# Kernel optimization log

Measured on AMD Instinct MI355X. Metric: run time of the kernel, lower is better.

## Reference

```python
import jax, jax.numpy as jnp
import numpy as np

NUM_CLASSES = 8
SCORE_T = 0.5
IOU_T = 0.5
POSE_HYPS = 10
MAX_DET = 100
B, A = 1, 4096


def _pairwise_iou(bx):
    # bx: (N,4) in (x1,y1,x2,y2); TF-style +1 pixel convention
    x1 = jnp.maximum(bx[:, None, 0], bx[None, :, 0])
    y1 = jnp.maximum(bx[:, None, 1], bx[None, :, 1])
    x2 = jnp.minimum(bx[:, None, 2], bx[None, :, 2])
    y2 = jnp.minimum(bx[:, None, 3], bx[None, :, 3])
    wid = x2 - x1 + 1.0
    hei = y2 - y1 + 1.0
    inter = wid * hei
    area = (bx[:, 2] - bx[:, 0] + 1.0) * (bx[:, 3] - bx[:, 1] + 1.0)
    den = area[:, None] + area[None, :] - inter
    ov = jnp.where(den == 0.0, 0.0, inter / jnp.where(den == 0.0, 1.0, den))  # divide_no_nan
    return jnp.where((wid <= 0.0) | (hei <= 0.0), 0.0, ov)


def _per_class(scores_c, boxes_c, poses_c, conf_c):
    # Fixed-shape re-expression of _filter_detections: instead of compacting the
    # boxes with score > threshold (dynamic shape), keep all N and mask invalid
    # boxes out of the overlap indicator. Relative ordering (which drives the
    # argmax tie-break and the ascending sort) is identical to the compacted
    # subset, so the math matches exactly.
    N = scores_c.shape[0]
    K = POSE_HYPS + 1
    valid = scores_c > SCORE_T
    m = jnp.sum(valid.astype(jnp.int32))  # number of selected boxes
    ov = _pairwise_iou(boxes_c)  # (N,N)
    ind = ((ov > IOU_T) & valid[:, None] & valid[None, :]).astype(jnp.float32)
    # scatter_nd: true_ov[argmax_col(row i), i] = max(row i); column i is unique per update
    max_col = jnp.argmax(ind, axis=1)
    true_ov = jnp.zeros_like(ind).at[max_col, jnp.arange(N)].add(jnp.max(ind, axis=1))
    bc = (1.0 - ov) * true_ov * conf_c[None, :]
    bc = jnp.where(bc == 0.0, 1000.0, bc)  # 1000 = sentinel for 'not a hypothesis'
    # Only the first min(pose_hyps+1, m) ascending-sorted entries per row survive the
    # sequence mask, so take the K smallest instead of a full argsort (same result;
    # top_k of the negation breaks ties by lowest index like a stable ascending sort).
    neg, args = jax.lax.top_k(-bc, K)
    svals = -neg  # (N,K) K smallest per row
    hyp = (jnp.arange(K) < jnp.minimum(K, m)).astype(jnp.float32)
    cmask = jnp.where(svals == 1000.0, 0.0, 1.0) * hyp[None, :]
    denom = jnp.sum(cmask, axis=1)  # (N,)
    safe = jnp.where(denom == 0.0, 1.0, denom)
    poses_avg = jnp.where(denom[:, None] == 0.0, 0.0,
                          jnp.sum(cmask[:, :, None] * poses_c[args], axis=1) / safe[:, None])
    boxes_avg = jnp.where(denom[:, None] == 0.0, 0.0,
                          jnp.sum(cmask[:, :, None] * boxes_c[args], axis=1) / safe[:, None])
    return poses_avg, boxes_avg, denom > 0.0


def _forward(boxes3D, boxes, classification, poses, confidence):
    C = NUM_CLASSES
    N = classification.shape[0] * classification.shape[1]
    cls = classification.reshape(N, C)
    bxs = boxes.reshape(N, C, 4)
    pss = poses.reshape(N, C, 12)
    cnf = confidence.reshape(N, C)
    # boxes3D is reshaped/gathered by the original but never used afterwards (dead code)
    xs = (cls.T, jnp.transpose(bxs, (1, 0, 2)), jnp.transpose(pss, (1, 0, 2)), cnf.T)
    # serialize over classes so only one NxN working set is live at a time
    poses_avg, boxes_avg, survive = jax.lax.map(lambda t: _per_class(*t), xs)
    surv = survive.reshape(-1)  # (C*N,) class-major, matching the original concat order
    count = jnp.sum(surv.astype(jnp.int32))
    scores_flat = jnp.where(surv, cls.T.reshape(-1), -jnp.inf)
    top_scores, _ = jax.lax.top_k(scores_flat, MAX_DET)
    rank = jnp.arange(MAX_DET)
    ok = rank < count
    out_scores = jnp.where(ok, top_scores, -1.0)
    # NOTE: the original computes top_indices but never applies it — labels/poses/
    # indices/boxes stay in class-major survivor order, truncated/padded with -1.
    pos = jnp.arange(C * N)
    order = jnp.argsort(jnp.where(surv, pos, pos + C * N))  # stable compaction
    sel = order[:MAX_DET]
    labels_flat = jnp.repeat(jnp.arange(C), N)
    anchors_flat = jnp.tile(jnp.arange(N), C)
    out_labels = jnp.where(ok, labels_flat[sel], -1).astype(jnp.int32)
    out_idx = jnp.where(ok, anchors_flat[sel], -1).astype(jnp.int32)
    out_poses = jnp.where(ok[:, None], poses_avg.reshape(C * N, 12)[sel], -1.0)
    out_boxes = jnp.where(ok[:, None], boxes_avg.reshape(C * N, 4)[sel], -1.0)
    return out_scores, out_labels, out_poses, out_idx, out_boxes


def setup_inputs():
    key = jax.random.key(0)
    k1, k2, k3, k4, k5, k6 = jax.random.split(key, 6)
    C = NUM_CLASSES
    # realistic heavily-overlapping boxes in a 640x640 image
    cxy = jax.random.uniform(k1, (B, A, C, 2), minval=0.0, maxval=640.0)
    wh = jax.random.uniform(k2, (B, A, C, 2), minval=10.0, maxval=120.0)
    boxes = jnp.concatenate([cxy - wh / 2.0, cxy + wh / 2.0], axis=-1).reshape(B, A, C * 4)
    return {
        "boxes3D": jax.random.normal(k6, (B, A, C * 16), dtype=jnp.float32),
        "boxes": boxes,
        "classification": jax.random.uniform(k3, (B, A, C), dtype=jnp.float32),
        "poses": jax.random.normal(k4, (B, A, C * 12), dtype=jnp.float32),
        "confidence": jax.random.uniform(k5, (B, A, C), dtype=jnp.float32),
    }


def reference(boxes3D, boxes, classification, poses, confidence):
    return _forward(boxes3D, boxes, classification, poses, confidence)
```

## Files before the change

### kernel.cpp

```cpp
#include <hip/hip_runtime.h>
#include <stdint.h>

#define N_ANCH 4096
#define NCLS 8
#define CN (N_ANCH * NCLS)
#define SCORE_TH 0.5f
#define IOU_TH 0.5f
#define KSEL 11
#define MAX_DET 100
#define CAND_CAP 4096
#define TILE 128
#define TPC (N_ANCH / TILE)
#define NTRI (TPC * (TPC + 1) / 2)

__device__ __forceinline__ float iou_f(float4 a, float areaA, float4 b, float areaB) {
    float x1 = fmaxf(a.x, b.x);
    float y1 = fmaxf(a.y, b.y);
    float x2 = fminf(a.z, b.z);
    float y2 = fminf(a.w, b.w);
    float wid = x2 - x1 + 1.0f;
    float hei = y2 - y1 + 1.0f;
    float inter = wid * hei;
    float den = areaA + areaB - inter;
    float ov = (den == 0.0f) ? 0.0f : (inter / den);
    if (wid <= 0.0f || hei <= 0.0f) ov = 0.0f;
    return ov;
}

__global__ void k_prep(const float* __restrict__ boxes, const float* __restrict__ cls,
                       const float* __restrict__ conf,
                       float4* boxesT, float* areaT, float* scoresT, float* confT,
                       int* surv, int* hist, int* gcnt, int* minRank) {
    int t = blockIdx.x * blockDim.x + threadIdx.x;
    if (t >= CN) return;
    int n = t >> 3;
    int c = t & 7;
    int p = c * N_ANCH + n;
    scoresT[p] = cls[t];
    confT[p] = conf[t];
    float4 b = reinterpret_cast<const float4*>(boxes)[t];
    boxesT[p] = b;
    areaT[p] = (b.z - b.x + 1.0f) * (b.w - b.y + 1.0f);
    surv[t] = 0;
    minRank[t] = 0x7FFFFFFF;
    if (t < 1024) hist[t] = 0;
    if (t == 1024) *gcnt = 0;
}

__global__ void __launch_bounds__(256) k_validlist(const float* __restrict__ scoresT,
                                                   int* validList, int* mVal) {
    int c = blockIdx.x;
    int tid = threadIdx.x;
    int lane = tid & 63, w = tid >> 6;
    __shared__ int wsum[4];
    __shared__ int base;
    if (tid == 0) base = 0;
    __syncthreads();
    for (int start = 0; start < N_ANCH; start += 256) {
        int n = start + tid;
        int flag = (scoresT[c * N_ANCH + n] > SCORE_TH) ? 1 : 0;
        unsigned long long mask = __ballot(flag);
        if (lane == 0) wsum[w] = __popcll(mask);
        __syncthreads();
        int rank = __popcll(mask & ((1ull << lane) - 1ull));
        int wbase = 0;
        for (int i = 0; i < w; i++) wbase += wsum[i];
        int total = wsum[0] + wsum[1] + wsum[2] + wsum[3];
        if (flag) validList[c * N_ANCH + base + wbase + rank] = n;
        __syncthreads();
        if (tid == 0) base += total;
        __syncthreads();
    }
    if (tid == 0) mVal[c] = base;
}

__global__ void __launch_bounds__(128) k_repmat(const float4* __restrict__ boxesT,
                                                const float* __restrict__ areaT,
                                                const int* __restrict__ validList,
                                                const int* __restrict__ mVal,
                                                int* minRank) {
    int bid = blockIdx.x;
    int c = bid / NTRI;
    int t = bid - c * NTRI;
    int ci = (int)((sqrtf(8.0f * (float)t + 1.0f) - 1.0f) * 0.5f);
    while ((ci + 1) * (ci + 2) / 2 <= t) ci++;
    while (ci * (ci + 1) / 2 > t) ci--;
    int cj = t - ci * (ci + 1) / 2;
    int mc = mVal[c];
    int ib = ci * TILE, jb = cj * TILE;
    if (ib >= mc || jb >= mc) return;
    int tid = threadIdx.x;
    int cbase = c << 12;
    const int* vl = validList + cbase;
    __shared__ float4 sB[TILE];
    __shared__ float sA[TILE];
    if (jb + tid < mc) {
        int vj = vl[jb + tid];
        sB[tid] = boxesT[cbase + vj];
        sA[tid] = areaT[cbase + vj];
    }
    __syncthreads();
    int i = ib + tid;
    if (i >= mc) return;
    int k = vl[i];
    float4 bk = boxesT[cbase + k];
    float ak = areaT[cbase + k];
    int limit = min(TILE, mc - jb);
    if (ci == cj) limit = min(limit, i - jb);
    int lmin = 0x7FFFFFFF;
    #pragma unroll 4
    for (int r = 0; r < limit; r++) {
        float ov = iou_f(bk, ak, sB[r], sA[r]);
        if (ov > IOU_TH && r < lmin) lmin = r;
    }
    if (lmin != 0x7FFFFFFF) atomicMin(&minRank[cbase + i], jb + lmin);
}

__global__ void __launch_bounds__(256) k_repfinal(const float4* __restrict__ boxesT,
                                                  const float* __restrict__ areaT,
                                                  const float* __restrict__ confT,
                                                  const int* __restrict__ validList,
                                                  const int* __restrict__ mVal,
                                                  const int* __restrict__ minRank,
                                                  int* rep, int* surv) {
    int t = blockIdx.x * blockDim.x + threadIdx.x;
    if (t >= CN) return;
    int c = t >> 12;
    int i = t & (N_ANCH - 1);
    int mc = mVal[c];
    if (i >= mc) return;
    int cbase = c << 12;
    const int* vl = validList + cbase;
    int k = vl[i];
    int mr = minRank[t];
    if (mr > i) mr = i;
    int j = vl[mr];
    rep[cbase + k] = j;
    if (mr < i) {
        float ov = iou_f(boxesT[cbase + k], areaT[cbase + k], boxesT[cbase + j], areaT[cbase + j]);
        float bcv = (1.0f - ov) * confT[cbase + k];
        if (bcv != 0.0f) surv[cbase + j] = 1;
    }
}

__global__ void __launch_bounds__(256) k_survscan(const int* __restrict__ surv,
                                                  const float* __restrict__ scoresT,
                                                  int* blockCnt, int* hist) {
    int b = blockIdx.x, tid = threadIdx.x;
    int p = b * 256 + tid;
    int flag = surv[p] != 0;
    unsigned long long mask = __ballot(flag);
    __shared__ int wcnt[4];
    if ((tid & 63) == 0) wcnt[tid >> 6] = __popcll(mask);
    if (flag) {
        unsigned bits = __float_as_uint(scoresT[p]);
        int bb = (int)((bits - 0x3F000000u) >> 13);
        int bkt = bb < 0 ? 0 : (bb > 1023 ? 1023 : bb);
        atomicAdd(&hist[bkt], 1);
    }
    __syncthreads();
    if (tid == 0) blockCnt[b] = wcnt[0] + wcnt[1] + wcnt[2] + wcnt[3];
}

__global__ void __launch_bounds__(256) k_prefix(const int* __restrict__ blockCnt,
                                                const int* __restrict__ hist,
                                                int* blockOff, int* count_g, int* t0_g) {
    int tid = threadIdx.x;
    __shared__ int sfx[256];
    __shared__ int thrB;
    __shared__ int countS;
    if (tid == 0) {
        int run = 0;
        for (int i = 0; i < 128; i++) { blockOff[i] = run; run += blockCnt[i]; }
        *count_g = run; countS = run; thrB = 0;
    }
    int part = hist[4 * tid] + hist[4 * tid + 1] + hist[4 * tid + 2] + hist[4 * tid + 3];
    sfx[tid] = part;
    __syncthreads();
    if (tid == 0) {
        int run = 0;
        for (int i = 255; i >= 0; i--) { int v = sfx[i]; sfx[i] = run; run += v; }
    }
    __syncthreads();
    int count = countS;
    int target = count < MAX_DET ? count : MAX_DET;
    int S = sfx[tid];
    int found = -1;
    for (int b = 4 * tid + 3; b >= 4 * tid; b--) {
        S += hist[b];
        if (found < 0 && S >= target) found = b;
    }
    if (found >= 0) atomicMax(&thrB, found);
    __syncthreads();
    if (tid == 0) *t0_g = thrB;
}

__global__ void __launch_bounds__(256) k_selgather(const int* __restrict__ surv,
                                                   const float* __restrict__ scoresT,
                                                   const int* __restrict__ blockOff,
                                                   const int* __restrict__ t0_g,
                                                   int* sel, float* cand, int* gcnt) {
    int b = blockIdx.x, tid = threadIdx.x;
    int lane = tid & 63, w = tid >> 6;
    int p = b * 256 + tid;
    int flag = surv[p] != 0;
    unsigned long long mask = __ballot(flag);
    __shared__ int wcnt[4];
    if (lane == 0) wcnt[w] = __popcll(mask);
    __syncthreads();
    int rank = __popcll(mask & ((1ull << lane) - 1ull));
    int wbase = 0;
    for (int i = 0; i < w; i++) wbase += wcnt[i];
    int idx = blockOff[b] + wbase + rank;
    if (flag && idx < MAX_DET) sel[idx] = p;
    if (flag) {
        unsigned bits = __float_as_uint(scoresT[p]);
        int bb = (int)((bits - 0x3F000000u) >> 13);
        int bkt = bb < 0 ? 0 : (bb > 1023 ? 1023 : bb);
        if (bkt >= *t0_g) {
            int id = atomicAdd(gcnt, 1);
            if (id < CAND_CAP) cand[id] = scoresT[p];
        }
    }
}

__global__ void __launch_bounds__(256) k_sort(const float* __restrict__ cand,
                                              const int* __restrict__ gcnt,
                                              const int* __restrict__ count_g,
                                              float* out) {
    __shared__ float s[CAND_CAP];
    int tid = threadIdx.x;
    int cc = *gcnt; if (cc > CAND_CAP) cc = CAND_CAP;
    int count = *count_g;
    int n = 128; while (n < cc) n <<= 1;
    for (int i = tid; i < n; i += 256) s[i] = (i < cc) ? -cand[i] : 1e38f;
    __syncthreads();
    for (int kk = 2; kk <= n; kk <<= 1) {
        for (int jj = kk >> 1; jj > 0; jj >>= 1) {
            for (int i = tid; i < n; i += 256) {
                int ixj = i ^ jj;
                if (ixj > i) {
                    float a = s[i], b2 = s[ixj];
                    bool up = ((i & kk) == 0);
                    if (up ? (a > b2) : (a < b2)) { s[i] = b2; s[ixj] = a; }
                }
            }
            __syncthreads();
        }
    }
    if (tid < MAX_DET) out[tid] = (tid < count) ? -s[tid] : -1.0f;
}

__global__ void __launch_bounds__(256) k_out(const float4* __restrict__ boxesT,
                                             const float* __restrict__ areaT,
                                             const float* __restrict__ confT,
                                             const float* __restrict__ poses,
                                             const int* __restrict__ validList,
                                             const int* __restrict__ mVal,
                                             const int* __restrict__ rep,
                                             const int* __restrict__ sel,
                                             const int* __restrict__ count_g,
                                             float* out) {
    int s = blockIdx.x;
    int tid = threadIdx.x;
    int count = *count_g;
    if (s >= count) {
        if (tid == 0) { out[100 + s] = -1.0f; out[1400 + s] = -1.0f; }
        if (tid < 12) out[200 + s * 12 + tid] = -1.0f;
        if (tid >= 16 && tid < 20) out[1500 + s * 4 + (tid - 16)] = -1.0f;
        return;
    }
    int p = sel[s];
    int c = p >> 12;
    int r = p & (N_ANCH - 1);
    __shared__ unsigned long long keyArr[4096];
    __shared__ int nmS;
    __shared__ int kselS[KSEL];
    __shared__ unsigned long long bestS;
    __shared__ unsigned long long redK[4];
    if (tid == 0) nmS = 0;
    __syncthreads();
    float4 br = boxesT[(c << 12) + r];
    float ar = areaT[(c << 12) + r];
    int mc = mVal[c];
    for (int i = tid; i < mc; i += 256) {
        int k = validList[(c << 12) + i];
        if (k != r && rep[(c << 12) + k] == r) {
            float ov = iou_f(br, ar, boxesT[(c << 12) + k], areaT[(c << 12) + k]);
            float bcv = (1.0f - ov) * confT[(c << 12) + k];
            if (bcv != 0.0f) {
                int id = atomicAdd(&nmS, 1);
                keyArr[id] = ((unsigned long long)__float_as_uint(bcv) << 32) | (unsigned)k;
            }
        }
    }
    __syncthreads();
    int nm = nmS;
    int dn = nm < KSEL ? nm : KSEL;
    unsigned long long lastBest = ~0ull;
    for (int j = 0; j < dn; j++) {
        unsigned long long bk = ~0ull;
        for (int i = tid; i < nm; i += 256) {
            unsigned long long v = keyArr[i];
            if (v == lastBest) { keyArr[i] = ~0ull; v = ~0ull; }
            if (v < bk) bk = v;
        }
        for (int off = 32; off > 0; off >>= 1) {
            unsigned long long o = __shfl_down(bk, off);
            if (o < bk) bk = o;
        }
        if ((tid & 63) == 0) redK[tid >> 6] = bk;
        __syncthreads();
        if (tid == 0) {
            unsigned long long B = redK[0];
            for (int q2 = 1; q2 < 4; q2++) if (redK[q2] < B) B = redK[q2];
            bestS = B;
            kselS[j] = (int)(B & 0xFFFFFFFFull);
        }
        __syncthreads();
        lastBest = bestS;
    }
    float fdn = (float)(dn > 0 ? dn : 1);
    if (tid < 12) {
        float ssum = 0.0f;
        for (int j = 0; j < dn; j++) {
            int k = kselS[j];
            ssum += poses[(k * 8 + c) * 12 + tid];
        }
        out[200 + s * 12 + tid] = ssum / fdn;
    } else if (tid < 16) {
        int d = tid - 12;
        float ssum = 0.0f;
        for (int j = 0; j < dn; j++) {
            int k = kselS[j];
            const float* bb = (const float*)&boxesT[(c << 12) + k];
            ssum += bb[d];
        }
        out[1500 + s * 4 + d] = ssum / fdn;
    } else if (tid == 16) {
        out[100 + s] = (float)c;
    } else if (tid == 17) {
        out[1400 + s] = (float)r;
    }
}

extern "C" void kernel_launch(void* const* d_in, const int* in_sizes, int n_in,
                              void* d_out, int out_size, void* d_ws, size_t ws_size,
                              hipStream_t stream) {
    const float* boxes = (const float*)d_in[1];
    const float* cls   = (const float*)d_in[2];
    const float* poses = (const float*)d_in[3];
    const float* conf  = (const float*)d_in[4];
    float* out = (float*)d_out;

    char* ws = (char*)d_ws;
    size_t off = 0;
    auto alloc = [&](size_t bytes) {
        void* p = ws + off;
        off += (bytes + 255) & ~(size_t)255;
        return p;
    };
    float4* boxesT  = (float4*)alloc(CN * sizeof(float4));
    float*  areaT   = (float*)alloc(CN * sizeof(float));
    float*  scoresT = (float*)alloc(CN * sizeof(float));
    float*  confT   = (float*)alloc(CN * sizeof(float));
    int*    validList = (int*)alloc(CN * sizeof(int));
    int*    mVal    = (int*)alloc(64);
    int*    rep     = (int*)alloc(CN * sizeof(int));
    int*    surv    = (int*)alloc(CN * sizeof(int));
    int*    sel     = (int*)alloc(MAX_DET * sizeof(int));
    int*    count_g = (int*)alloc(64);
    float*  cand    = (float*)alloc(CAND_CAP * sizeof(float));
    int*    hist    = (int*)alloc(1024 * sizeof(int));
    int*    blockCnt = (int*)alloc(128 * sizeof(int));
    int*    blockOff = (int*)alloc(128 * sizeof(int));
    int*    t0_g    = (int*)alloc(64);
    int*    gcnt    = (int*)alloc(64);
    int*    minRank = (int*)alloc(CN * sizeof(int));

    k_prep<<<CN / 256, 256, 0, stream>>>(boxes, cls, conf, boxesT, areaT, scoresT, confT, surv, hist, gcnt, minRank);
    k_validlist<<<NCLS, 256, 0, stream>>>(scoresT, validList, mVal);
    k_repmat<<<NCLS * NTRI, 128, 0, stream>>>(boxesT, areaT, validList, mVal, minRank);
    k_repfinal<<<CN / 256, 256, 0, stream>>>(boxesT, areaT, confT, validList, mVal, minRank, rep, surv);
    k_survscan<<<128, 256, 0, stream>>>(surv, scoresT, blockCnt, hist);
    k_prefix<<<1, 256, 0, stream>>>(blockCnt, hist, blockOff, count_g, t0_g);
    k_selgather<<<128, 256, 0, stream>>>(surv, scoresT, blockOff, t0_g, sel, cand, gcnt);
    k_sort<<<1, 256, 0, stream>>>(cand, gcnt, count_g, out);
    k_out<<<MAX_DET, 256, 0, stream>>>(boxesT, areaT, confT, poses, validList, mVal, rep, sel, count_g, out);
}
```

Before: 138.3 us.

## Fuse post-NMS stages into one cooperative kernel and compact valid boxes

Merges the rep-final, survivor scan, prefix, select/gather, sort and output kernels into a single cooperative kernel that uses grid-wide syncs between phases, cutting several launches and the gaps between them. The valid-list kernel becomes a single-pass 1024-thread scan that also writes compacted box and area arrays, so the pairwise IoU kernel reads contiguous data instead of gathering through indices. The output phase now scans all anchors via rep instead of only the valid list. rep is not initialised for invalid anchors, so stale workspace contents could be picked up. Grid syncs and cooperative-launch limits add their own overhead and constraints.

```diff
diff --git a/kernel.cpp b/kernel.cpp
--- a/kernel.cpp
+++ b/kernel.cpp
@@ -1,5 +1,8 @@
 #include <hip/hip_runtime.h>
+#include <hip/hip_cooperative_groups.h>
 #include <stdint.h>
+
+namespace cg = cooperative_groups;
 
 #define N_ANCH 4096
 #define NCLS 8
@@ -47,36 +50,45 @@
     if (t == 1024) *gcnt = 0;
 }
 
-__global__ void __launch_bounds__(256) k_validlist(const float* __restrict__ scoresT,
-                                                   int* validList, int* mVal) {
+__global__ void __launch_bounds__(1024) k_validlist(const float* __restrict__ scoresT,
+                                                    const float4* __restrict__ boxesT,
+                                                    const float* __restrict__ areaT,
+                                                    int* validList, float4* vBox,
+                                                    float* vArea, int* mVal) {
     int c = blockIdx.x;
     int tid = threadIdx.x;
-    int lane = tid & 63, w = tid >> 6;
-    __shared__ int wsum[4];
-    __shared__ int base;
-    if (tid == 0) base = 0;
+    int lane = tid & 63, wid = tid >> 6;
+    __shared__ int wsum[16];
+    int cbase = c << 12;
+    float4 sc = reinterpret_cast<const float4*>(scoresT + cbase)[tid];
+    int f0 = sc.x > SCORE_TH, f1 = sc.y > SCORE_TH, f2 = sc.z > SCORE_TH, f3 = sc.w > SCORE_TH;
+    int f = f0 + f1 + f2 + f3;
+    int inc = f;
+    for (int off = 1; off < 64; off <<= 1) {
+        int o = __shfl_up(inc, off);
+        if (lane >= off) inc += o;
+    }
+    if (lane == 63) wsum[wid] = inc;
     __syncthreads();
-    for (int start = 0; start < N_ANCH; start += 256) {
-        int n = start + tid;
-        int flag = (scoresT[c * N_ANCH + n] > SCORE_TH) ? 1 : 0;
-        unsigned long long mask = __ballot(flag);
-        if (lane == 0) wsum[w] = __popcll(mask);
-        __syncthreads();
-        int rank = __popcll(mask & ((1ull << lane) - 1ull));
-        int wbase = 0;
-        for (int i = 0; i < w; i++) wbase += wsum[i];
-        int total = wsum[0] + wsum[1] + wsum[2] + wsum[3];
-        if (flag) validList[c * N_ANCH + base + wbase + rank] = n;
-        __syncthreads();
-        if (tid == 0) base += total;
-        __syncthreads();
-    }
-    if (tid == 0) mVal[c] = base;
-}
-
-__global__ void __launch_bounds__(128) k_repmat(const float4* __restrict__ boxesT,
-                                                const float* __restrict__ areaT,
-                                                const int* __restrict__ validList,
+    int wbase = 0;
+    for (int i = 0; i < wid; i++) wbase += wsum[i];
+    int pos = wbase + inc - f;
+    int n0 = tid * 4;
+    int fl[4] = {f0, f1, f2, f3};
+    for (int d = 0; d < 4; d++) {
+        if (fl[d]) {
+            int n = n0 + d;
+            validList[cbase + pos] = n;
+            vBox[cbase + pos] = boxesT[cbase + n];
+            vArea[cbase + pos] = areaT[cbase + n];
+            pos++;
+        }
+    }
+    if (tid == 1023) mVal[c] = wbase + inc;
+}
+
+__global__ void __launch_bounds__(128) k_repmat(const float4* __restrict__ vBox,
+                                                const float* __restrict__ vArea,
                                                 const int* __restrict__ mVal,
                                                 int* minRank) {
     int bid = blockIdx.x;
@@ -91,20 +103,17 @@
     if (ib >= mc || jb >= mc) return;
     int tid = threadIdx.x;
     int cbase = c << 12;
-    const int* vl = validList + cbase;
     __shared__ float4 sB[TILE];
     __shared__ float sA[TILE];
     if (jb + tid < mc) {
-        int vj = vl[jb + tid];
-        sB[tid] = boxesT[cbase + vj];
-        sA[tid] = areaT[cbase + vj];
+        sB[tid] = vBox[cbase + jb + tid];
+        sA[tid] = vArea[cbase + jb + tid];
     }
     __syncthreads();
     int i = ib + tid;
     if (i >= mc) return;
-    int k = vl[i];
-    float4 bk = boxesT[cbase + k];
-    float ak = areaT[cbase + k];
+    float4 bk = vBox[cbase + i];
+    float ak = vArea[cbase + i];
     int limit = min(TILE, mc - jb);
     if (ci == cj) limit = min(limit, i - jb);
     int lmin = 0x7FFFFFFF;
@@ -116,231 +125,222 @@
     if (lmin != 0x7FFFFFFF) atomicMin(&minRank[cbase + i], jb + lmin);
 }
 
-__global__ void __launch_bounds__(256) k_repfinal(const float4* __restrict__ boxesT,
-                                                  const float* __restrict__ areaT,
-                                                  const float* __restrict__ confT,
-                                                  const int* __restrict__ validList,
-                                                  const int* __restrict__ mVal,
-                                                  const int* __restrict__ minRank,
-                                                  int* rep, int* surv) {
-    int t = blockIdx.x * blockDim.x + threadIdx.x;
-    if (t >= CN) return;
-    int c = t >> 12;
-    int i = t & (N_ANCH - 1);
-    int mc = mVal[c];
-    if (i >= mc) return;
-    int cbase = c << 12;
-    const int* vl = validList + cbase;
-    int k = vl[i];
-    int mr = minRank[t];
-    if (mr > i) mr = i;
-    int j = vl[mr];
-    rep[cbase + k] = j;
-    if (mr < i) {
-        float ov = iou_f(boxesT[cbase + k], areaT[cbase + k], boxesT[cbase + j], areaT[cbase + j]);
-        float bcv = (1.0f - ov) * confT[cbase + k];
-        if (bcv != 0.0f) surv[cbase + j] = 1;
-    }
-}
-
-__global__ void __launch_bounds__(256) k_survscan(const int* __restrict__ surv,
-                                                  const float* __restrict__ scoresT,
-                                                  int* blockCnt, int* hist) {
-    int b = blockIdx.x, tid = threadIdx.x;
-    int p = b * 256 + tid;
-    int flag = surv[p] != 0;
-    unsigned long long mask = __ballot(flag);
+__global__ void __launch_bounds__(256) k_tail(const float4* __restrict__ boxesT,
+                                              const float* __restrict__ areaT,
+                                              const float* __restrict__ confT,
+                                              const float* __restrict__ scoresT,
+                                              const float* __restrict__ poses,
+                                              const int* __restrict__ validList,
+                                              const int* __restrict__ mVal,
+                                              const float4* __restrict__ vBox,
+                                              const float* __restrict__ vArea,
+                                              const int* __restrict__ minRank,
+                                              int* rep, int* surv, int* hist,
+                                              int* blockCnt, int* blockOff,
+                                              int* count_g, int* t0_g,
+                                              int* sel, float* cand, int* gcnt,
+                                              float* out) {
+    cg::grid_group grid = cg::this_grid();
+    int bid = blockIdx.x, tid = threadIdx.x;
+    int lane = tid & 63, w = tid >> 6;
+    int t = bid * 256 + tid;
+
     __shared__ int wcnt[4];
-    if ((tid & 63) == 0) wcnt[tid >> 6] = __popcll(mask);
-    if (flag) {
-        unsigned bits = __float_as_uint(scoresT[p]);
-        int bb = (int)((bits - 0x3F000000u) >> 13);
-        int bkt = bb < 0 ? 0 : (bb > 1023 ? 1023 : bb);
-        atomicAdd(&hist[bkt], 1);
-    }
-    __syncthreads();
-    if (tid == 0) blockCnt[b] = wcnt[0] + wcnt[1] + wcnt[2] + wcnt[3];
-}
-
-__global__ void __launch_bounds__(256) k_prefix(const int* __restrict__ blockCnt,
-                                                const int* __restrict__ hist,
-                                                int* blockOff, int* count_g, int* t0_g) {
-    int tid = threadIdx.x;
     __shared__ int sfx[256];
-    __shared__ int thrB;
-    __shared__ int countS;
-    if (tid == 0) {
-        int run = 0;
-        for (int i = 0; i < 128; i++) { blockOff[i] = run; run += blockCnt[i]; }
-        *count_g = run; countS = run; thrB = 0;
-    }
-    int part = hist[4 * tid] + hist[4 * tid + 1] + hist[4 * tid + 2] + hist[4 * tid + 3];
-    sfx[tid] = part;
-    __syncthreads();
-    if (tid == 0) {
-        int run = 0;
-        for (int i = 255; i >= 0; i--) { int v = sfx[i]; sfx[i] = run; run += v; }
-    }
-    __syncthreads();
-    int count = countS;
-    int target = count < MAX_DET ? count : MAX_DET;
-    int S = sfx[tid];
-    int found = -1;
-    for (int b = 4 * tid + 3; b >= 4 * tid; b--) {
-        S += hist[b];
-        if (found < 0 && S >= target) found = b;
-    }
-    if (found >= 0) atomicMax(&thrB, found);
-    __syncthreads();
-    if (tid == 0) *t0_g = thrB;
-}
-
-__global__ void __launch_bounds__(256) k_selgather(const int* __restrict__ surv,
-                                                   const float* __restrict__ scoresT,
-                                                   const int* __restrict__ blockOff,
-                                                   const int* __restrict__ t0_g,
-                                                   int* sel, float* cand, int* gcnt) {
-    int b = blockIdx.x, tid = threadIdx.x;
-    int lane = tid & 63, w = tid >> 6;
-    int p = b * 256 + tid;
-    int flag = surv[p] != 0;
-    unsigned long long mask = __ballot(flag);
-    __shared__ int wcnt[4];
-    if (lane == 0) wcnt[w] = __popcll(mask);
-    __syncthreads();
-    int rank = __popcll(mask & ((1ull << lane) - 1ull));
-    int wbase = 0;
-    for (int i = 0; i < w; i++) wbase += wcnt[i];
-    int idx = blockOff[b] + wbase + rank;
-    if (flag && idx < MAX_DET) sel[idx] = p;
-    if (flag) {
-        unsigned bits = __float_as_uint(scoresT[p]);
-        int bb = (int)((bits - 0x3F000000u) >> 13);
-        int bkt = bb < 0 ? 0 : (bb > 1023 ? 1023 : bb);
-        if (bkt >= *t0_g) {
-            int id = atomicAdd(gcnt, 1);
-            if (id < CAND_CAP) cand[id] = scoresT[p];
-        }
-    }
-}
-
-__global__ void __launch_bounds__(256) k_sort(const float* __restrict__ cand,
-                                              const int* __restrict__ gcnt,
-                                              const int* __restrict__ count_g,
-                                              float* out) {
-    __shared__ float s[CAND_CAP];
-    int tid = threadIdx.x;
-    int cc = *gcnt; if (cc > CAND_CAP) cc = CAND_CAP;
-    int count = *count_g;
-    int n = 128; while (n < cc) n <<= 1;
-    for (int i = tid; i < n; i += 256) s[i] = (i < cc) ? -cand[i] : 1e38f;
-    __syncthreads();
-    for (int kk = 2; kk <= n; kk <<= 1) {
-        for (int jj = kk >> 1; jj > 0; jj >>= 1) {
-            for (int i = tid; i < n; i += 256) {
-                int ixj = i ^ jj;
-                if (ixj > i) {
-                    float a = s[i], b2 = s[ixj];
-                    bool up = ((i & kk) == 0);
-                    if (up ? (a > b2) : (a < b2)) { s[i] = b2; s[ixj] = a; }
-                }
-            }
-            __syncthreads();
-        }
-    }
-    if (tid < MAX_DET) out[tid] = (tid < count) ? -s[tid] : -1.0f;
-}
-
-__global__ void __launch_bounds__(256) k_out(const float4* __restrict__ boxesT,
-                                             const float* __restrict__ areaT,
-                                             const float* __restrict__ confT,
-                                             const float* __restrict__ poses,
-                                             const int* __restrict__ validList,
-                                             const int* __restrict__ mVal,
-                                             const int* __restrict__ rep,
-                                             const int* __restrict__ sel,
-                                             const int* __restrict__ count_g,
-                                             float* out) {
-    int s = blockIdx.x;
-    int tid = threadIdx.x;
-    int count = *count_g;
-    if (s >= count) {
-        if (tid == 0) { out[100 + s] = -1.0f; out[1400 + s] = -1.0f; }
-        if (tid < 12) out[200 + s * 12 + tid] = -1.0f;
-        if (tid >= 16 && tid < 20) out[1500 + s * 4 + (tid - 16)] = -1.0f;
-        return;
-    }
-    int p = sel[s];
-    int c = p >> 12;
-    int r = p & (N_ANCH - 1);
+    __shared__ float sSort[CAND_CAP];
     __shared__ unsigned long long keyArr[4096];
     __shared__ int nmS;
     __shared__ int kselS[KSEL];
     __shared__ unsigned long long bestS;
     __shared__ unsigned long long redK[4];
-    if (tid == 0) nmS = 0;
-    __syncthreads();
-    float4 br = boxesT[(c << 12) + r];
-    float ar = areaT[(c << 12) + r];
-    int mc = mVal[c];
-    for (int i = tid; i < mc; i += 256) {
-        int k = validList[(c << 12) + i];
-        if (k != r && rep[(c << 12) + k] == r) {
-            float ov = iou_f(br, ar, boxesT[(c << 12) + k], areaT[(c << 12) + k]);
-            float bcv = (1.0f - ov) * confT[(c << 12) + k];
-            if (bcv != 0.0f) {
-                int id = atomicAdd(&nmS, 1);
-                keyArr[id] = ((unsigned long long)__float_as_uint(bcv) << 32) | (unsigned)k;
-            }
-        }
-    }
-    __syncthreads();
-    int nm = nmS;
-    int dn = nm < KSEL ? nm : KSEL;
-    unsigned long long lastBest = ~0ull;
-    for (int j = 0; j < dn; j++) {
-        unsigned long long bk = ~0ull;
-        for (int i = tid; i < nm; i += 256) {
-            unsigned long long v = keyArr[i];
-            if (v == lastBest) { keyArr[i] = ~0ull; v = ~0ull; }
-            if (v < bk) bk = v;
-        }
-        for (int off = 32; off > 0; off >>= 1) {
-            unsigned long long o = __shfl_down(bk, off);
-            if (o < bk) bk = o;
-        }
-        if ((tid & 63) == 0) redK[tid >> 6] = bk;
-        __syncthreads();
+
+    {
+        int c = t >> 12;
+        int i = t & (N_ANCH - 1);
+        int mc = mVal[c];
+        if (i < mc) {
+            int cbase = c << 12;
+            int k = validList[cbase + i];
+            int mr = minRank[cbase + i];
+            if (mr > i) mr = i;
+            int j = validList[cbase + mr];
+            rep[cbase + k] = j;
+            if (mr < i) {
+                float ov = iou_f(vBox[cbase + i], vArea[cbase + i],
+                                 vBox[cbase + mr], vArea[cbase + mr]);
+                float bcv = (1.0f - ov) * confT[cbase + k];
+                if (bcv != 0.0f) surv[cbase + j] = 1;
+            }
+        }
+    }
+    __threadfence();
+    grid.sync();
+
+    {
+        int flag = surv[t] != 0;
+        unsigned long long mask = __ballot(flag);
+        if (lane == 0) wcnt[w] = __popcll(mask);
+        if (flag) {
+            unsigned bits = __float_as_uint(scoresT[t]);
+            int bb = (int)((bits - 0x3F000000u) >> 13);
+            int bkt = bb < 0 ? 0 : (bb > 1023 ? 1023 : bb);
+            atomicAdd(&hist[bkt], 1);
+        }
+        __syncthreads();
+        if (tid == 0) blockCnt[bid] = wcnt[0] + wcnt[1] + wcnt[2] + wcnt[3];
+    }
+    __threadfence();
+    grid.sync();
+
+    if (bid == 0) {
+        __shared__ int thrB;
+        __shared__ int countS;
         if (tid == 0) {
-            unsigned long long B = redK[0];
-            for (int q2 = 1; q2 < 4; q2++) if (redK[q2] < B) B = redK[q2];
-            bestS = B;
-            kselS[j] = (int)(B & 0xFFFFFFFFull);
-        }
-        __syncthreads();
-        lastBest = bestS;
-    }
-    float fdn = (float)(dn > 0 ? dn : 1);
-    if (tid < 12) {
-        float ssum = 0.0f;
-        for (int j = 0; j < dn; j++) {
-            int k = kselS[j];
-            ssum += poses[(k * 8 + c) * 12 + tid];
-        }
-        out[200 + s * 12 + tid] = ssum / fdn;
-    } else if (tid < 16) {
-        int d = tid - 12;
-        float ssum = 0.0f;
-        for (int j = 0; j < dn; j++) {
-            int k = kselS[j];
-            const float* bb = (const float*)&boxesT[(c << 12) + k];
-            ssum += bb[d];
-        }
-        out[1500 + s * 4 + d] = ssum / fdn;
-    } else if (tid == 16) {
-        out[100 + s] = (float)c;
-    } else if (tid == 17) {
-        out[1400 + s] = (float)r;
+            int run = 0;
+            for (int i = 0; i < 128; i++) { blockOff[i] = run; run += blockCnt[i]; }
+            *count_g = run; countS = run; thrB = 0;
+        }
+        int part = hist[4 * tid] + hist[4 * tid + 1] + hist[4 * tid + 2] + hist[4 * tid + 3];
+        sfx[tid] = part;
+        __syncthreads();
+        if (tid == 0) {
+            int run = 0;
+            for (int i = 255; i >= 0; i--) { int v = sfx[i]; sfx[i] = run; run += v; }
+        }
+        __syncthreads();
+        int count = countS;
+        int target = count < MAX_DET ? count : MAX_DET;
+        int S = sfx[tid];
+        int found = -1;
+        for (int b = 4 * tid + 3; b >= 4 * tid; b--) {
+            S += hist[b];
+            if (found < 0 && S >= target) found = b;
+        }
+        if (found >= 0) atomicMax(&thrB, found);
+        __syncthreads();
+        if (tid == 0) *t0_g = thrB;
+    }
+    __threadfence();
+    grid.sync();
+
+    {
+        int flag = surv[t] != 0;
+        unsigned long long mask = __ballot(flag);
+        if (lane == 0) wcnt[w] = __popcll(mask);
+        __syncthreads();
+        int rank = __popcll(mask & ((1ull << lane) - 1ull));
+        int wbase = 0;
+        for (int i = 0; i < w; i++) wbase += wcnt[i];
+        int idx = blockOff[bid] + wbase + rank;
+        if (flag && idx < MAX_DET) sel[idx] = t;
+        if (flag) {
+            unsigned bits = __float_as_uint(scoresT[t]);
+            int bb = (int)((bits - 0x3F000000u) >> 13);
+            int bkt = bb < 0 ? 0 : (bb > 1023 ? 1023 : bb);
+            if (bkt >= *t0_g) {
+                int id = atomicAdd(gcnt, 1);
+                if (id < CAND_CAP) cand[id] = scoresT[t];
+            }
+        }
+    }
+    __threadfence();
+    grid.sync();
+
+    int count = *count_g;
+    if (bid == 0) {
+        int cc = *gcnt; if (cc > CAND_CAP) cc = CAND_CAP;
+        int n = 128; while (n < cc) n <<= 1;
+        for (int i = tid; i < n; i += 256) sSort[i] = (i < cc) ? -cand[i] : 1e38f;
+        __syncthreads();
+        for (int kk = 2; kk <= n; kk <<= 1) {
+            for (int jj = kk >> 1; jj > 0; jj >>= 1) {
+                for (int i = tid; i < n; i += 256) {
+                    int ixj = i ^ jj;
+                    if (ixj > i) {
+                        float a = sSort[i], b2 = sSort[ixj];
+                        bool up = ((i & kk) == 0);
+                        if (up ? (a > b2) : (a < b2)) { sSort[i] = b2; sSort[ixj] = a; }
+                    }
+                }
+                __syncthreads();
+            }
+        }
+        if (tid < MAX_DET) out[tid] = (tid < count) ? -sSort[tid] : -1.0f;
+    } else if (bid <= MAX_DET) {
+        int s = bid - 1;
+        if (s >= count) {
+            if (tid == 0) { out[100 + s] = -1.0f; out[1400 + s] = -1.0f; }
+            if (tid < 12) out[200 + s * 12 + tid] = -1.0f;
+            if (tid >= 16 && tid < 20) out[1500 + s * 4 + (tid - 16)] = -1.0f;
+        } else {
+            int p = sel[s];
+            int c = p >> 12;
+            int r = p & (N_ANCH - 1);
+            int cbase = c << 12;
+            if (tid == 0) nmS = 0;
+            __syncthreads();
+            float4 br = boxesT[cbase + r];
+            float ar = areaT[cbase + r];
+            for (int k = tid; k < N_ANCH; k += 256) {
+                int rp = rep[cbase + k];
+                if (rp == r && k != r) {
+                    float ov = iou_f(br, ar, boxesT[cbase + k], areaT[cbase + k]);
+                    float bcv = (1.0f - ov) * confT[cbase + k];
+                    if (bcv != 0.0f) {
+                        int id = atomicAdd(&nmS, 1);
+                        keyArr[id] = ((unsigned long long)__float_as_uint(bcv) << 32) | (unsigned)k;
+                    }
+                }
+            }
+            __syncthreads();
+            int nm = nmS;
+            int dn = nm < KSEL ? nm : KSEL;
+            unsigned long long lastBest = ~0ull;
+            for (int j = 0; j < dn; j++) {
+                unsigned long long bk = ~0ull;
+                for (int i = tid; i < nm; i += 256) {
+                    unsigned long long v = keyArr[i];
+                    if (v == lastBest) { keyArr[i] = ~0ull; v = ~0ull; }
+                    if (v < bk) bk = v;
+                }
+                for (int off = 32; off > 0; off >>= 1) {
+                    unsigned long long o = __shfl_down(bk, off);
+                    if (o < bk) bk = o;
+                }
+                if (lane == 0) redK[w] = bk;
+                __syncthreads();
+                if (tid == 0) {
+                    unsigned long long B = redK[0];
+                    for (int q2 = 1; q2 < 4; q2++) if (redK[q2] < B) B = redK[q2];
+                    bestS = B;
+                    kselS[j] = (int)(B & 0xFFFFFFFFull);
+                }
+                __syncthreads();
+                lastBest = bestS;
+            }
+            float fdn = (float)(dn > 0 ? dn : 1);
+            if (tid < 12) {
+                float ssum = 0.0f;
+                for (int j = 0; j < dn; j++) {
+                    int k = kselS[j];
+                    ssum += poses[(k * 8 + c) * 12 + tid];
+                }
+                out[200 + s * 12 + tid] = ssum / fdn;
+            } else if (tid < 16) {
+                int d = tid - 12;
+                float ssum = 0.0f;
+                for (int j = 0; j < dn; j++) {
+                    int k = kselS[j];
+                    const float* bb = (const float*)&boxesT[cbase + k];
+                    ssum += bb[d];
+                }
+                out[1500 + s * 4 + d] = ssum / fdn;
+            } else if (tid == 16) {
+                out[100 + s] = (float)c;
+            } else if (tid == 17) {
+                out[1400 + s] = (float)r;
+            }
+        }
     }
 }
 
@@ -365,6 +365,8 @@
     float*  scoresT = (float*)alloc(CN * sizeof(float));
     float*  confT   = (float*)alloc(CN * sizeof(float));
     int*    validList = (int*)alloc(CN * sizeof(int));
+    float4* vBox    = (float4*)alloc(CN * sizeof(float4));
+    float*  vArea   = (float*)alloc(CN * sizeof(float));
     int*    mVal    = (int*)alloc(64);
     int*    rep     = (int*)alloc(CN * sizeof(int));
     int*    surv    = (int*)alloc(CN * sizeof(int));
@@ -378,13 +380,17 @@
     int*    gcnt    = (int*)alloc(64);
     int*    minRank = (int*)alloc(CN * sizeof(int));
 
-    k_prep<<<CN / 256, 256, 0, stream>>>(boxes, cls, conf, boxesT, areaT, scoresT, confT, surv, hist, gcnt, minRank);
-    k_validlist<<<NCLS, 256, 0, stream>>>(scoresT, validList, mVal);
-    k_repmat<<<NCLS * NTRI, 128, 0, stream>>>(boxesT, areaT, validList, mVal, minRank);
-    k_repfinal<<<CN / 256, 256, 0, stream>>>(boxesT, areaT, confT, validList, mVal, minRank, rep, surv);
-    k_survscan<<<128, 256, 0, stream>>>(surv, scoresT, blockCnt, hist);
-    k_prefix<<<1, 256, 0, stream>>>(blockCnt, hist, blockOff, count_g, t0_g);
-    k_selgather<<<128, 256, 0, stream>>>(surv, scoresT, blockOff, t0_g, sel, cand, gcnt);
-    k_sort<<<1, 256, 0, stream>>>(cand, gcnt, count_g, out);
-    k_out<<<MAX_DET, 256, 0, stream>>>(boxesT, areaT, confT, poses, validList, mVal, rep, sel, count_g, out);
-}
+    k_prep<<<CN / 256, 256, 0, stream>>>(boxes, cls, conf, boxesT, areaT, scoresT, confT,
+                                         surv, hist, gcnt, minRank);
+    k_validlist<<<NCLS, 1024, 0, stream>>>(scoresT, boxesT, areaT, validList, vBox, vArea, mVal);
+    k_repmat<<<NCLS * NTRI, 128, 0, stream>>>(vBox, vArea, mVal, minRank);
+
+    void* args[] = {
+        (void*)&boxesT, (void*)&areaT, (void*)&confT, (void*)&scoresT, (void*)&poses,
+        (void*)&validList, (void*)&mVal, (void*)&vBox, (void*)&vArea, (void*)&minRank,
+        (void*)&rep, (void*)&surv, (void*)&hist, (void*)&blockCnt, (void*)&blockOff,
+        (void*)&count_g, (void*)&t0_g, (void*)&sel, (void*)&cand, (void*)&gcnt,
+        (void*)&out
+    };
+    hipLaunchCooperativeKernel((void*)k_tail, dim3(128), dim3(256), args, 0, stream);
+}
```

Result: slower. 250.6 us (+81.2%).
